# Performance work log

Measured on AMD Instinct MI355X. Metric: run time of the kernel, lower is better.

## Reference

```python
import jax, jax.numpy as jnp
import numpy as np

GROUPS = 32
EPS = 1e-5
NUM_HEADS = 8

def group_norm(x, scale, bias):
    # x: [N, C, T], GroupNorm(32) as in diffusion normalization()
    N, C, T = x.shape
    xg = x.reshape(N, GROUPS, -1)
    mean = xg.mean(-1, keepdims=True)
    var = xg.var(-1, keepdims=True)
    xg = (xg - mean) * jax.lax.rsqrt(var + EPS)
    return xg.reshape(N, C, T) * scale[None, :, None] + bias[None, :, None]


def setup_inputs() -> dict:
    key = jax.random.key(0)
    ks = jax.random.split(key, 10)
    B, D, C, T, TE = 2, 32, 256, 64, 1024
    s = 0.02
    inp = {}
    inp["x"] = jax.random.normal(ks[0], (B, D, C, T), jnp.float32)
    inp["temb"] = jax.random.normal(ks[1], (B, TE, T), jnp.float32)
    inp["frame_indices"] = jnp.sort(jax.random.randint(ks[2], (B, T), 0, 1000), axis=-1)
    inp["attn_mask"] = jnp.ones((B, T), jnp.float32)
    inp["norm_scale"] = jnp.ones((C,), jnp.float32)
    inp["norm_bias"] = jnp.zeros((C,), jnp.float32)
    inp["w_qkv"] = jax.random.normal(ks[3], (3 * C, C), jnp.float32) * s
    inp["b_qkv"] = jnp.zeros((3 * C,), jnp.float32)
    inp["w_aug1"] = jax.random.normal(ks[4], (C, 3), jnp.float32) * s
    inp["b_aug1"] = jnp.zeros((C,), jnp.float32)
    inp["w_aug2"] = jax.random.normal(ks[5], (C, TE), jnp.float32) * s
    inp["b_aug2"] = jnp.zeros((C,), jnp.float32)
    inp["w_aug3"] = jax.random.normal(ks[6], (C, C), jnp.float32) * s
    inp["b_aug3"] = jnp.zeros((C,), jnp.float32)
    inp["w_proj"] = jax.random.normal(ks[7], (C, C), jnp.float32) * s
    inp["b_proj"] = jnp.zeros((C,), jnp.float32)
    return inp


def reference(x, temb, frame_indices, attn_mask, norm_scale, norm_bias,
              w_qkv, b_qkv, w_aug1, b_aug1, w_aug2, b_aug2, w_aug3, b_aug3,
              w_proj, b_proj):
    B, D, C, T = x.shape
    H = NUM_HEADS
    cph = C // H  # channels per head
    # norm + 1x1 qkv conv over channels
    h = group_norm(x.reshape(B * D, C, T), norm_scale, norm_bias)
    qkv = jnp.einsum('nct,oc->not', h, w_qkv) + b_qkv[None, :, None]
    qkv = qkv.reshape(B, D, 3, cph, H, T)
    q, k, v = qkv[:, :, 0], qkv[:, :, 1], qkv[:, :, 2]
    scale = 1.0 / np.sqrt(np.sqrt(cph))
    w = jnp.einsum('bdcht,bdchs->bdhts', q * scale, k * scale)  # [B,D,H,T,T]
    # relative-position features: [B,3,T,T]
    rel = frame_indices[:, None, None, :] - frame_indices[:, None, :, None]
    rel3 = jnp.concatenate([
        jnp.clip(rel, 0, None).astype(jnp.float32),
        jnp.clip(-rel, 0, None).astype(jnp.float32),
        (rel == 0).astype(jnp.float32)], axis=1)
    rel3 = jnp.log1p(rel3)
    emb = jnp.einsum('bits,oi->bots', rel3, w_aug1) + b_aug1[None, :, None, None]  # [B,C,T,T]
    emb = emb + (jnp.einsum('bet,oe->bot', temb, w_aug2) + b_aug2[None, :, None])[:, :, :, None]
    wa = jnp.einsum('bits,oi->bots', jax.nn.relu(emb), w_aug3) + b_aug3[None, :, None, None]
    # tile heads into full channel dim (matches torch .repeat ordering) and add bias pre-softmax
    w = jnp.tile(w, (1, 1, cph, 1, 1)) + wa[:, None]  # [B,D,C,T,T]
    w = jnp.where(attn_mask[:, None, None, None, :] > 0, w, -jnp.inf)
    w = jax.nn.softmax(w.astype(jnp.float32), axis=-1).astype(x.dtype)
    hv = jnp.einsum('bdcts,bdcs->bdct', w, v.reshape(B, D, C, T))
    out = x + jnp.einsum('bdct,oc->bdot', hv, w_proj) + b_proj[None, None, :, None]
    return out
```

## Files before the change

kernel.cpp:

```cpp
#include <hip/hip_runtime.h>

#define B_ 2
#define D_ 32
#define C_ 256
#define T_ 64
#define TE_ 1024
#define H_ 8
#define N_ 64

typedef __attribute__((ext_vector_type(8))) short bf16x8;
typedef __attribute__((ext_vector_type(8))) unsigned short u16x8;
typedef __attribute__((ext_vector_type(4))) float f32x4;

__device__ inline ushort f2bf(float x){
  unsigned u = __float_as_uint(x);
  unsigned r = u + 0x7FFFu + ((u>>16)&1u);
  return (ushort)(r>>16);
}
__device__ inline float bf2f(ushort u){
  return __uint_as_float(((unsigned)u)<<16);
}

__global__ __launch_bounds__(256) void k_prep(
    const float* __restrict__ w_qkv, const float* __restrict__ wp,
    const float* __restrict__ w3,
    ushort* __restrict__ wqb, ushort* __restrict__ wpb, ushort* __restrict__ w3b,
    const float* __restrict__ x, const float* __restrict__ nsc,
    const float* __restrict__ nbi, ushort* __restrict__ ht,
    const float* __restrict__ temb, const float* __restrict__ w2,
    const float* __restrict__ b2, float* __restrict__ tp)
{
  __shared__ float smem[5120];
  int blk = blockIdx.x;
  int tid = threadIdx.x;
  if (blk < 320) {
    const float* src; ushort* dst; int n4, i0;
    if (blk < 192)      { src = w_qkv; dst = wqb; n4 = 49152; i0 = blk; }
    else if (blk < 256) { src = wp;    dst = wpb; n4 = 16384; i0 = blk-192; }
    else                { src = w3;    dst = w3b; n4 = 16384; i0 = blk-256; }
    int i = i0*256 + tid;
    if (i < n4){
      float4 v = ((const float4*)src)[i];
      ushort4 o; o.x=f2bf(v.x); o.y=f2bf(v.y); o.z=f2bf(v.z); o.w=f2bf(v.w);
      ((ushort4*)dst)[i] = o;
    }
    return;
  }
  if (blk < 2368) {
    int b2k = blk - 320;
    int n = b2k >> 5, g = b2k & 31;
    const float* xp = x + ((size_t)n*C_ + g*8) * T_;
    float v0 = xp[tid], v1 = xp[tid+256];
    float s = v0+v1, ss = v0*v0 + v1*v1;
    #pragma unroll
    for (int off=32; off; off>>=1) { s += __shfl_down(s,off); ss += __shfl_down(ss,off); }
    float* red = smem;
    int wid = tid>>6, lane = tid&63;
    if (lane==0){ red[wid]=s; red[4+wid]=ss; }
    __syncthreads();
    if (tid==0){
      float a  = red[0]+red[1]+red[2]+red[3];
      float bb = red[4]+red[5]+red[6]+red[7];
      float mean = a*(1.f/512.f);
      float var  = bb*(1.f/512.f) - mean*mean;
      red[8]=mean; red[9]=rsqrtf(var + 1e-5f);
    }
    __syncthreads();
    float mean = red[8], inv = red[9];
    int t = tid & 63;
    int c0 = g*8 + (tid>>6), c1 = c0 + 4;
    size_t rowb = ((size_t)n*T_ + t)*C_;
    ht[rowb + c0] = f2bf((v0-mean)*inv*nsc[c0] + nbi[c0]);
    ht[rowb + c1] = f2bf((v1-mean)*inv*nsc[c1] + nbi[c1]);
    return;
  }
  {
    int b3k = blk - 2368;
    int b = b3k >> 6, ob = b3k & 63;
    float* w2s = smem;
    float* red = smem + 4096;
    const float* w2p = w2 + (size_t)ob*4*1024;
    #pragma unroll
    for (int r = 0; r < 16; r++) w2s[r*256 + tid] = w2p[r*256 + tid];
    __syncthreads();
    int t = tid & 63, eq = tid >> 6;
    const float* tep = temb + ((size_t)b*1024 + eq*256)*64 + t;
    const float* wq  = w2s + eq*256;
    float acc[4] = {0.f,0.f,0.f,0.f};
    #pragma unroll 4
    for (int i = 0; i < 256; i += 4) {
      float tv0 = tep[(i+0)*64];
      float tv1 = tep[(i+1)*64];
      float tv2 = tep[(i+2)*64];
      float tv3 = tep[(i+3)*64];
      #pragma unroll
      for (int j = 0; j < 4; j++) {
        float4 w4 = *(const float4*)&wq[j*1024 + i];
        acc[j] = fmaf(w4.x, tv0, acc[j]);
        acc[j] = fmaf(w4.y, tv1, acc[j]);
        acc[j] = fmaf(w4.z, tv2, acc[j]);
        acc[j] = fmaf(w4.w, tv3, acc[j]);
      }
    }
    #pragma unroll
    for (int j=0;j<4;j++) red[(eq*4+j)*64 + t] = acc[j];
    __syncthreads();
    if (tid < 64) {
      #pragma unroll
      for (int j=0;j<4;j++){
        int o = ob*4 + j;
        float v = red[j*64+tid]+red[(4+j)*64+tid]+red[(8+j)*64+tid]+red[(12+j)*64+tid];
        tp[((size_t)b*256+o)*64 + tid] = v + b2[o];
      }
    }
  }
}

__global__ __launch_bounds__(256) void k_mm(
    const ushort* __restrict__ Wb, const ushort* __restrict__ Inb,
    const float* __restrict__ bias, const float* __restrict__ resid,
    void* __restrict__ OutV, int oblocks, int Ototal, int mode)
{
  int blk = blockIdx.x;
  int n = blk / oblocks, ob = blk - n*oblocks;
  int tid = threadIdx.x;
  int lane = tid & 63, w = tid >> 6;
  int o0 = ob*64 + w*16;
  int r = lane & 15, kg = lane >> 4;
  const ushort* wp = Wb + (size_t)(o0 + r)*256 + kg*8;
  const ushort* ip = Inb + ((size_t)n*64 + r)*256 + kg*8;
  f32x4 acc[4];
  #pragma unroll
  for (int j=0;j<4;j++) acc[j] = (f32x4){0.f,0.f,0.f,0.f};
  #pragma unroll
  for (int ks = 0; ks < 8; ks++) {
    bf16x8 a = *(const bf16x8*)(wp + ks*32);
    #pragma unroll
    for (int j = 0; j < 4; j++) {
      bf16x8 b = *(const bf16x8*)(ip + (size_t)j*16*256 + ks*32);
      acc[j] = __builtin_amdgcn_mfma_f32_16x16x32_bf16(a, b, acc[j], 0, 0, 0);
    }
  }
  #pragma unroll
  for (int j = 0; j < 4; j++) {
    #pragma unroll
    for (int rr = 0; rr < 4; rr++) {
      int o = o0 + kg*4 + rr;
      size_t idx = ((size_t)n*Ototal + o)*64 + j*16 + r;
      float v = acc[j][rr] + bias[o];
      if (mode == 0) {
        v += resid[idx];
        ((float*)OutV)[idx] = v;
      } else {
        if (o < 512) v *= 0.42044820762685725f;
        ((ushort*)OutV)[idx] = f2bf(v);
      }
    }
  }
}

__global__ __launch_bounds__(256) void k_sw(
    const ushort* __restrict__ qkv, ushort* __restrict__ es,
    const float* __restrict__ amask,
    const int* __restrict__ fi, const float* __restrict__ w1,
    const float* __restrict__ b1, const float* __restrict__ tp,
    const ushort* __restrict__ w3b, const float* __restrict__ b3,
    ushort* __restrict__ ew)
{
  __shared__ char smem[33536];
  int blk = blockIdx.x;
  int tid = threadIdx.x;
  if (blk < 512) {
    int n = blk >> 3, hh = blk & 7;
    float* qs = (float*)smem;
    float* ks = qs + 2048;
    const ushort* base = qkv + (size_t)n*(768*64);
    for (int i=tid; i<2048; i+=256){
      int cq = i>>6, tt = i&63;
      qs[i] = bf2f(base[(cq*8+hh)*64 + tt]);
      ks[i] = bf2f(base[(256 + cq*8+hh)*64 + tt]);
    }
    __syncthreads();
    int s  = tid & 63;
    int t4 = __builtin_amdgcn_readfirstlane(tid>>6);
    float msk = amask[(n >> 5)*64 + s];
    float acc[16];
    #pragma unroll
    for (int j=0;j<16;j++) acc[j]=0.f;
    for (int cq=0;cq<32;cq++){
      float kv = ks[cq*64+s];
      #pragma unroll
      for (int j=0;j<16;j++) acc[j] = fmaf(qs[cq*64 + t4*16 + j], kv, acc[j]);
    }
    ushort* op = es + (size_t)blk*4096;
    #pragma unroll
    for (int j=0;j<16;j++)
      op[(t4*16+j)*64 + s] = f2bf(msk > 0.f ? __expf(acc[j]) : 0.f);
    return;
  }
  {
    int blk2 = blk - 512;
    int oh = blk2 & 1; int bt = blk2 >> 1;
    int b = bt >> 6, t = bt & 63;
    float* l0 = (float*)smem;
    float* l1 = l0 + 64;
    float* l2 = l1 + 64;
    ushort* Ebuf = (ushort*)(smem + 768);
    if (tid < 64){
      int rel = fi[b*64+tid] - fi[b*64+t];
      float r0 = rel>0 ? (float)rel   : 0.f;
      float r1 = rel<0 ? (float)(-rel): 0.f;
      l0[tid] = log1pf(r0);
      l1[tid] = log1pf(r1);
      l2[tid] = (rel==0) ? 0.6931471805599453f : 0.f;
    }
    __syncthreads();
    int s = tid & 63;
    int iq = __builtin_amdgcn_readfirstlane(tid >> 6);
    float L0 = l0[s], L1 = l1[s], L2 = l2[s];
    #pragma unroll
    for (int c8 = 0; c8 < 8; c8++){
      int chunk = iq*8 + c8;
      int ibase = chunk*8;
      u16x8 pack;
      #pragma unroll
      for (int e = 0; e < 8; e++){
        int i = ibase + e;
        float bb = b1[i] + tp[((size_t)b*256 + i)*64 + t];
        float evv = fmaf(w1[i*3], L0, fmaf(w1[i*3+1], L1, fmaf(w1[i*3+2], L2, bb)));
        pack[e] = f2bf(fmaxf(evv, 0.f));
      }
      int csw = chunk ^ (s & 31);
      *(u16x8*)&Ebuf[s*256 + csw*8] = pack;
    }
    __syncthreads();
    int lane = tid & 63, w = tid >> 6;
    int r = lane & 15, kg = lane >> 4;
    int o0 = oh*128 + w*32;
    f32x4 acc[2][4];
    #pragma unroll
    for (int m=0;m<2;m++)
      #pragma unroll
      for (int j=0;j<4;j++) acc[m][j] = (f32x4){0.f,0.f,0.f,0.f};
    #pragma unroll
    for (int ks8 = 0; ks8 < 8; ks8++){
      bf16x8 a0 = *(const bf16x8*)(w3b + (size_t)(o0 +      r)*256 + kg*8 + ks8*32);
      bf16x8 a1 = *(const bf16x8*)(w3b + (size_t)(o0 + 16 + r)*256 + kg*8 + ks8*32);
      #pragma unroll
      for (int j=0;j<4;j++){
        int srow = j*16 + r;
        int chunk = (kg + ks8*4) ^ (srow & 31);
        bf16x8 bfr = *(const bf16x8*)&Ebuf[srow*256 + chunk*8];
        acc[0][j] = __builtin_amdgcn_mfma_f32_16x16x32_bf16(a0, bfr, acc[0][j], 0, 0, 0);
        acc[1][j] = __builtin_amdgcn_mfma_f32_16x16x32_bf16(a1, bfr, acc[1][j], 0, 0, 0);
      }
    }
    #pragma unroll
    for (int m=0;m<2;m++){
      #pragma unroll
      for (int j=0;j<4;j++){
        #pragma unroll
        for (int rr=0;rr<4;rr++){
          int o = o0 + m*16 + kg*4 + rr;
          int scol = j*16 + r;
          ew[((size_t)(b*256+o))*4096 + t*64 + scol] = f2bf(__expf(acc[m][j][rr] + b3[o]));
        }
      }
    }
  }
}

__global__ __launch_bounds__(256) void k_attn(
    const ushort* __restrict__ es, const ushort* __restrict__ ew,
    const ushort* __restrict__ qkv, ushort* __restrict__ hv_t)
{
  int i = blockIdx.x;
  int xcd = i & 7, j0 = i >> 3;
  int g = xcd + ((j0 >> 6) << 3);
  int w64 = j0 & 63;
  int b = g >> 3, hh = g & 7;
  int dq = w64 >> 3, cs = w64 & 7;
  int tid = threadIdx.x;
  int t  = tid & 63;
  int dj = __builtin_amdgcn_readfirstlane(tid >> 6);
  int n  = b*D_ + dq*4 + dj;
  __shared__ float4 ewl[64][16];
  __shared__ float4 vl4[4][16];
  float4 esr[16];
  {
    const u16x8* sp = (const u16x8*)(es + ((size_t)(n*8 + hh))*4096 + (size_t)t*64);
    #pragma unroll
    for (int k8=0;k8<8;k8++){
      u16x8 e8 = sp[k8];
      float4 lo, hi;
      lo.x=bf2f(e8[0]); lo.y=bf2f(e8[1]); lo.z=bf2f(e8[2]); lo.w=bf2f(e8[3]);
      hi.x=bf2f(e8[4]); hi.y=bf2f(e8[5]); hi.z=bf2f(e8[6]); hi.w=bf2f(e8[7]);
      esr[2*k8] = lo; esr[2*k8+1] = hi;
    }
  }
  int vd = tid >> 4, vk = tid & 15;
  u16x8 rew[2]; ushort4 rv;
  {
    int c = cs*32 + hh;
    const u16x8* wap = (const u16x8*)(ew + ((size_t)(b*256 + c))*4096);
    rew[0] = wap[tid]; rew[1] = wap[tid+256];
    if (tid < 64)
      rv = *(const ushort4*)(qkv + ((size_t)(b*D_ + dq*4 + vd)*768 + 512 + c)*64 + 4*vk);
  }
  for (int ci=0; ci<4; ci++){
    __syncthreads();
    #pragma unroll
    for (int i2=0;i2<2;i2++){
      int ch = tid + 256*i2;
      int tr = ch >> 3, k8 = ch & 7;
      u16x8 e8 = rew[i2];
      float4 lo, hi;
      lo.x=bf2f(e8[0]); lo.y=bf2f(e8[1]); lo.z=bf2f(e8[2]); lo.w=bf2f(e8[3]);
      hi.x=bf2f(e8[4]); hi.y=bf2f(e8[5]); hi.z=bf2f(e8[6]); hi.w=bf2f(e8[7]);
      ewl[tr][(k8*2)   ^ (tr & 15)] = lo;
      ewl[tr][(k8*2+1) ^ (tr & 15)] = hi;
    }
    if (tid < 64){
      float4 vv; vv.x=bf2f(rv.x); vv.y=bf2f(rv.y); vv.z=bf2f(rv.z); vv.w=bf2f(rv.w);
      vl4[vd][vk] = vv;
    }
    __syncthreads();
    if (ci < 3){
      int c = (cs*4 + ci + 1)*8 + hh;
      const u16x8* wap = (const u16x8*)(ew + ((size_t)(b*256 + c))*4096);
      rew[0] = wap[tid]; rew[1] = wap[tid+256];
      if (tid < 64)
        rv = *(const ushort4*)(qkv + ((size_t)(b*D_ + dq*4 + vd)*768 + 512 + c)*64 + 4*vk);
    }
    float sum = 0.f;
    float ax=0.f, ay=0.f, az=0.f, aw=0.f;
    #pragma unroll
    for (int k=0;k<16;k++){
      float4 e4 = esr[k];
      float4 w4 = ewl[t][k ^ (t & 15)];
      float4 v4 = vl4[dj][k];
      float px = e4.x*w4.x, py = e4.y*w4.y, pz = e4.z*w4.z, pw = e4.w*w4.w;
      sum += px+py+pz+pw;
      ax = fmaf(px, v4.x, ax);
      ay = fmaf(py, v4.y, ay);
      az = fmaf(pz, v4.z, az);
      aw = fmaf(pw, v4.w, aw);
    }
    float acc = (ax+ay)+(az+aw);
    int c = (cs*4 + ci)*8 + hh;
    hv_t[((size_t)n*64 + t)*256 + c] = f2bf(acc / sum);
  }
}

extern "C" void kernel_launch(void* const* d_in, const int* in_sizes, int n_in,
                              void* d_out, int out_size, void* d_ws, size_t ws_size,
                              hipStream_t stream) {
  const float* x     = (const float*)d_in[0];
  const float* temb  = (const float*)d_in[1];
  const int*   fi    = (const int*)  d_in[2];
  const float* amask = (const float*)d_in[3];
  const float* nsc   = (const float*)d_in[4];
  const float* nbi   = (const float*)d_in[5];
  const float* w_qkv = (const float*)d_in[6];
  const float* b_qkv = (const float*)d_in[7];
  const float* w1    = (const float*)d_in[8];
  const float* b1    = (const float*)d_in[9];
  const float* w2    = (const float*)d_in[10];
  const float* b2    = (const float*)d_in[11];
  const float* w3    = (const float*)d_in[12];
  const float* b3    = (const float*)d_in[13];
  const float* wp    = (const float*)d_in[14];
  const float* bp    = (const float*)d_in[15];
  float* out = (float*)d_out;

  ushort* qkvb = (ushort*)d_ws;
  float*  tpb  = (float*)(qkvb + 3145728);
  ushort* esb  = (ushort*)(tpb + 32768);
  ushort* ewb  = esb + 2097152;
  ushort* htb  = ewb + 2097152;
  ushort* hvb  = htb + 1048576;
  ushort* wqb  = hvb + 1048576;
  ushort* wpb  = wqb + 196608;
  ushort* w3b  = wpb + 65536;

  k_prep <<<2496, 256, 0, stream>>>(w_qkv, wp, w3, wqb, wpb, w3b,
                                    x, nsc, nbi, htb, temb, w2, b2, tpb);
  k_mm   <<<N_*12, 256, 0, stream>>>(wqb, htb, b_qkv, nullptr, qkvb, 12, 768, 1);
  k_sw   <<<768, 256, 0, stream>>>(qkvb, esb, amask, fi, w1, b1, tpb, w3b, b3, ewb);
  k_attn <<<B_*H_*8*8, 256, 0, stream>>>(esb, ewb, qkvb, hvb);
  k_mm   <<<N_*4,  256, 0, stream>>>(wpb, hvb, bp, x, out, 4, 256, 0);
}
```

Before: 75.56 us.

## Coalesce attention output and norm stores; permute proj weights to match new layout

The attention kernel now writes its output in a [n][head][channel-quad][t] layout with t contiguous, instead of scattering 2-byte stores at a stride of 256 elements. To keep the output projection correct, the projection weight columns are permuted in the prep kernel, and a dedicated k_proj kernel gathers the B fragments with 8 strided loads. The group-norm store is also staged through shared memory, so each thread writes one 16-byte vector instead of scattered shorts. The trade-off is cheaper stores in the attention and norm stages against less efficient strided loads in the projection GEMM, plus an extra barrier in the norm path.

```diff
diff --git a/kernel.cpp b/kernel.cpp
--- a/kernel.cpp
+++ b/kernel.cpp
@@ -24,7 +24,7 @@
 __global__ __launch_bounds__(256) void k_prep(
     const float* __restrict__ w_qkv, const float* __restrict__ wp,
     const float* __restrict__ w3,
-    ushort* __restrict__ wqb, ushort* __restrict__ wpb, ushort* __restrict__ w3b,
+    ushort* __restrict__ wqb, ushort* __restrict__ wpr, ushort* __restrict__ w3b,
     const float* __restrict__ x, const float* __restrict__ nsc,
     const float* __restrict__ nbi, ushort* __restrict__ ht,
     const float* __restrict__ temb, const float* __restrict__ w2,
@@ -34,15 +34,26 @@
   int blk = blockIdx.x;
   int tid = threadIdx.x;
   if (blk < 320) {
-    const float* src; ushort* dst; int n4, i0;
-    if (blk < 192)      { src = w_qkv; dst = wqb; n4 = 49152; i0 = blk; }
-    else if (blk < 256) { src = wp;    dst = wpb; n4 = 16384; i0 = blk-192; }
-    else                { src = w3;    dst = w3b; n4 = 16384; i0 = blk-256; }
-    int i = i0*256 + tid;
-    if (i < n4){
-      float4 v = ((const float4*)src)[i];
+    if (blk < 192) {
+      int i = blk*256 + tid;
+      float4 v = ((const float4*)w_qkv)[i];
       ushort4 o; o.x=f2bf(v.x); o.y=f2bf(v.y); o.z=f2bf(v.z); o.w=f2bf(v.w);
-      ((ushort4*)dst)[i] = o;
+      ((ushort4*)wqb)[i] = o;
+    } else if (blk < 256) {
+      int i = (blk-192)*256 + tid;
+      float4 v = ((const float4*)wp)[i];
+      int o = i >> 6, c0 = (i & 63)*4;
+      #pragma unroll
+      for (int e=0;e<4;e++){
+        int c = c0+e;
+        float vv = (e==0)?v.x:(e==1)?v.y:(e==2)?v.z:v.w;
+        wpr[o*256 + (c&7)*32 + (c>>3)] = f2bf(vv);
+      }
+    } else {
+      int i = (blk-256)*256 + tid;
+      float4 v = ((const float4*)w3)[i];
+      ushort4 o; o.x=f2bf(v.x); o.y=f2bf(v.y); o.z=f2bf(v.z); o.w=f2bf(v.w);
+      ((ushort4*)w3b)[i] = o;
     }
     return;
   }
@@ -55,6 +66,7 @@
     #pragma unroll
     for (int off=32; off; off>>=1) { s += __shfl_down(s,off); ss += __shfl_down(ss,off); }
     float* red = smem;
+    ushort* gbuf = (ushort*)(smem + 16);
     int wid = tid>>6, lane = tid&63;
     if (lane==0){ red[wid]=s; red[4+wid]=ss; }
     __syncthreads();
@@ -67,11 +79,17 @@
     }
     __syncthreads();
     float mean = red[8], inv = red[9];
-    int t = tid & 63;
-    int c0 = g*8 + (tid>>6), c1 = c0 + 4;
-    size_t rowb = ((size_t)n*T_ + t)*C_;
-    ht[rowb + c0] = f2bf((v0-mean)*inv*nsc[c0] + nbi[c0]);
-    ht[rowb + c1] = f2bf((v1-mean)*inv*nsc[c1] + nbi[c1]);
+    int t = tid & 63, w = tid >> 6;
+    int c0 = g*8 + w, c1 = c0 + 4;
+    gbuf[w*64 + t]     = f2bf((v0-mean)*inv*nsc[c0] + nbi[c0]);
+    gbuf[(w+4)*64 + t] = f2bf((v1-mean)*inv*nsc[c1] + nbi[c1]);
+    __syncthreads();
+    if (tid < 64){
+      u16x8 pk;
+      #pragma unroll
+      for (int i=0;i<8;i++) pk[i] = gbuf[i*64 + tid];
+      *(u16x8*)&ht[((size_t)n*T_ + tid)*C_ + g*8] = pk;
+    }
     return;
   }
   {
@@ -118,11 +136,10 @@
 
 __global__ __launch_bounds__(256) void k_mm(
     const ushort* __restrict__ Wb, const ushort* __restrict__ Inb,
-    const float* __restrict__ bias, const float* __restrict__ resid,
-    void* __restrict__ OutV, int oblocks, int Ototal, int mode)
+    const float* __restrict__ bias, ushort* __restrict__ Out)
 {
   int blk = blockIdx.x;
-  int n = blk / oblocks, ob = blk - n*oblocks;
+  int n = blk / 12, ob = blk - n*12;
   int tid = threadIdx.x;
   int lane = tid & 63, w = tid >> 6;
   int o0 = ob*64 + w*16;
@@ -146,15 +163,10 @@
     #pragma unroll
     for (int rr = 0; rr < 4; rr++) {
       int o = o0 + kg*4 + rr;
-      size_t idx = ((size_t)n*Ototal + o)*64 + j*16 + r;
+      size_t idx = ((size_t)n*768 + o)*64 + j*16 + r;
       float v = acc[j][rr] + bias[o];
-      if (mode == 0) {
-        v += resid[idx];
-        ((float*)OutV)[idx] = v;
-      } else {
-        if (o < 512) v *= 0.42044820762685725f;
-        ((ushort*)OutV)[idx] = f2bf(v);
-      }
+      if (o < 512) v *= 0.42044820762685725f;
+      Out[idx] = f2bf(v);
     }
   }
 }
@@ -272,7 +284,7 @@
 
 __global__ __launch_bounds__(256) void k_attn(
     const ushort* __restrict__ es, const ushort* __restrict__ ew,
-    const ushort* __restrict__ qkv, ushort* __restrict__ hv_t)
+    const ushort* __restrict__ qkv, ushort* __restrict__ hv1)
 {
   int i = blockIdx.x;
   int xcd = i & 7, j0 = i >> 3;
@@ -347,8 +359,46 @@
       aw = fmaf(pw, v4.w, aw);
     }
     float acc = (ax+ay)+(az+aw);
-    int c = (cs*4 + ci)*8 + hh;
-    hv_t[((size_t)n*64 + t)*256 + c] = f2bf(acc / sum);
+    int cq = cs*4 + ci;
+    hv1[(((size_t)n*8 + hh)*32 + cq)*64 + t] = f2bf(acc / sum);
+  }
+}
+
+__global__ __launch_bounds__(256) void k_proj(
+    const ushort* __restrict__ Wr, const ushort* __restrict__ hv1,
+    const float* __restrict__ bias, const float* __restrict__ resid,
+    float* __restrict__ Out)
+{
+  int blk = blockIdx.x;
+  int n = blk >> 2, ob = blk & 3;
+  int tid = threadIdx.x;
+  int lane = tid & 63, w = tid >> 6;
+  int o0 = ob*64 + w*16;
+  int r = lane & 15, kg = lane >> 4;
+  const ushort* wp = Wr + (size_t)(o0 + r)*256 + kg*8;
+  f32x4 acc[4];
+  #pragma unroll
+  for (int j=0;j<4;j++) acc[j] = (f32x4){0.f,0.f,0.f,0.f};
+  #pragma unroll
+  for (int ks = 0; ks < 8; ks++) {
+    bf16x8 a = *(const bf16x8*)(wp + ks*32);
+    #pragma unroll
+    for (int j = 0; j < 4; j++) {
+      const ushort* bp = hv1 + (((size_t)n*8 + ks)*32 + kg*8)*64 + (j*16 + r);
+      bf16x8 bfr;
+      #pragma unroll
+      for (int e=0;e<8;e++) bfr[e] = (short)bp[(size_t)e*64];
+      acc[j] = __builtin_amdgcn_mfma_f32_16x16x32_bf16(a, bfr, acc[j], 0, 0, 0);
+    }
+  }
+  #pragma unroll
+  for (int j = 0; j < 4; j++) {
+    #pragma unroll
+    for (int rr = 0; rr < 4; rr++) {
+      int o = o0 + kg*4 + rr;
+      size_t idx = ((size_t)n*256 + o)*64 + j*16 + r;
+      Out[idx] = acc[j][rr] + bias[o] + resid[idx];
+    }
   }
 }
 
@@ -380,13 +430,13 @@
   ushort* htb  = ewb + 2097152;
   ushort* hvb  = htb + 1048576;
   ushort* wqb  = hvb + 1048576;
-  ushort* wpb  = wqb + 196608;
-  ushort* w3b  = wpb + 65536;
-
-  k_prep <<<2496, 256, 0, stream>>>(w_qkv, wp, w3, wqb, wpb, w3b,
+  ushort* wprb = wqb + 196608;
+  ushort* w3b  = wprb + 65536;
+
+  k_prep <<<2496, 256, 0, stream>>>(w_qkv, wp, w3, wqb, wprb, w3b,
                                     x, nsc, nbi, htb, temb, w2, b2, tpb);
-  k_mm   <<<N_*12, 256, 0, stream>>>(wqb, htb, b_qkv, nullptr, qkvb, 12, 768, 1);
+  k_mm   <<<N_*12, 256, 0, stream>>>(wqb, htb, b_qkv, qkvb);
   k_sw   <<<768, 256, 0, stream>>>(qkvb, esb, amask, fi, w1, b1, tpb, w3b, b3, ewb);
   k_attn <<<B_*H_*8*8, 256, 0, stream>>>(esb, ewb, qkvb, hvb);
-  k_mm   <<<N_*4,  256, 0, stream>>>(wpb, hvb, bp, x, out, 4, 256, 0);
-}
+  k_proj <<<N_*4, 256, 0, stream>>>(wprb, hvb, bp, x, out);
+}
```

After: 64.49 us. -14.6%, faster.
